# Kernel tuning notes

Measured on AMD Instinct MI355X. Metric: run time of the kernel, lower is better.

## Reference

```python
import jax, jax.numpy as jnp
import numpy as np

D, E, H, K = 1024, 8, 4096, 2
B, S = 4, 2048


def setup_inputs() -> dict:
    key = jax.random.key(0)
    ks = jax.random.split(key, 5)
    scale = 0.02
    return {
        "x": jax.random.normal(ks[0], (B, S, D), dtype=jnp.float32),
        "gate_w": jax.random.normal(ks[1], (D, E), dtype=jnp.float32) * scale,
        "w1": jax.random.normal(ks[2], (E, D, H), dtype=jnp.float32) * scale,
        "b1": jnp.zeros((E, H), dtype=jnp.float32),
        "w2": jax.random.normal(ks[3], (E, H, D), dtype=jnp.float32) * scale,
        "b2": jnp.zeros((E, D), dtype=jnp.float32),
        "top_k": K,
    }


def reference(x, gate_w, w1, b1, w2, b2, top_k):
    orig_shape = x.shape
    d = x.shape[-1]
    xt = x.reshape(-1, d)                      # [T, D]
    T = xt.shape[0]

    # Gating: top-k over expert scores, softmax over the selected k.
    scores = xt @ gate_w                       # [T, E]
    expert_weights, expert_indices = jax.lax.top_k(scores, top_k)  # [T, K]
    expert_weights = jax.nn.softmax(expert_weights, axis=-1)

    # Dense all-expert MLP (GPT-style fc -> GELU -> proj), batched over experts.
    h = jnp.einsum('td,edh->eth', xt, w1) + b1[:, None, :]   # [E, T, H]
    h = jax.nn.gelu(h, approximate=False)
    outs = jnp.einsum('eth,ehd->etd', h, w2) + b2[:, None, :]  # [E, T, D]

    # Combine: gather each token's selected experts and mix with gate weights.
    tok = jnp.arange(T)[:, None]               # [T, 1]
    gathered = outs[expert_indices, tok]       # [T, K, D]
    y = jnp.sum(gathered * expert_weights[..., None], axis=1)  # [T, D]
    return y.reshape(orig_shape)
```

## Files before the change

### kernel.cpp

```cpp
#include <hip/hip_runtime.h>
#include <stdint.h>

#define T_TOK 8192
#define D_DIM 1024
#define E_NUM 8
#define H_DIM 4096

#define BM 128
#define BN 128
#define BK 64
#define NSEG 8
#define MAX_ROWS2 17408
#define MAX_MT2 (MAX_ROWS2/BM)
#define LCS 136

typedef unsigned short u16;
typedef __attribute__((ext_vector_type(8))) short shortx8;
typedef __attribute__((ext_vector_type(4))) float floatx4;
typedef __attribute__((ext_vector_type(8))) unsigned short ushortx8;

typedef const __attribute__((address_space(1))) unsigned int g_uint;
typedef __attribute__((address_space(3))) unsigned int l_uint;

__device__ __forceinline__ u16 f2bf(float f) {
  union { float f; unsigned int u; } v; v.f = f;
  unsigned int r = v.u + 0x7FFFu + ((v.u >> 16) & 1u);
  return (u16)(r >> 16);
}
__device__ __forceinline__ void gld_lds16(const u16* g, u16* l) {
  __builtin_amdgcn_global_load_lds((g_uint*)g, (l_uint*)l, 16, 0, 0);
}
__device__ __forceinline__ float gelu_fast(float v) {
  float y = v * (1.5957691216f + 0.07135481627f * v * v);
  y = fminf(y, 30.f);
  float ey = __expf(y);
  return v * ey * __builtin_amdgcn_rcpf(1.f + ey);
}

__global__ __launch_bounds__(256) void init_kernel(int* counts, int* fills, int* row_token) {
  int i = blockIdx.x * 256 + threadIdx.x;
  if (i < MAX_ROWS2) row_token[i] = -1;
  if (blockIdx.x == 0 && threadIdx.x < NSEG) { counts[threadIdx.x] = 0; fills[threadIdx.x] = 0; }
}

__global__ __launch_bounds__(256) void zero4_kernel(float4* out) {
  out[(size_t)blockIdx.x * 256 + threadIdx.x] = float4{0.f, 0.f, 0.f, 0.f};
}

__global__ __launch_bounds__(256) void gate_kernel(const float* __restrict__ X, const float* __restrict__ GW,
                                                   u16* __restrict__ XC,
                                                   int* __restrict__ tk_idx, float* __restrict__ tk_w,
                                                   int* __restrict__ counts) {
  const int lane = threadIdx.x & 63;
  const int t = blockIdx.x * 4 + (threadIdx.x >> 6);
  const float4* xr4 = (const float4*)(X + (size_t)t * D_DIM + lane * 16);
  const float4* gw4 = (const float4*)GW;
  float acc[E_NUM];
#pragma unroll
  for (int e = 0; e < E_NUM; e++) acc[e] = 0.f;
  ushortx8 o0, o1;
#pragma unroll
  for (int i4 = 0; i4 < 4; i4++) {
    float4 xv = xr4[i4];
#pragma unroll
    for (int c = 0; c < 4; c++) {
      float xs = (&xv.x)[c];
      int q = i4 * 4 + c;
      if (q < 8) o0[q] = f2bf(xs); else o1[q - 8] = f2bf(xs);
      int d = lane * 16 + q;
      float4 g0 = gw4[d * 2], g1 = gw4[d * 2 + 1];
      acc[0] += xs * g0.x; acc[1] += xs * g0.y; acc[2] += xs * g0.z; acc[3] += xs * g0.w;
      acc[4] += xs * g1.x; acc[5] += xs * g1.y; acc[6] += xs * g1.z; acc[7] += xs * g1.w;
    }
  }
  u16* xcb = XC + (size_t)t * D_DIM + lane * 16;
  *(ushortx8*)xcb = o0;
  *(ushortx8*)(xcb + 8) = o1;
#pragma unroll
  for (int e = 0; e < E_NUM; e++)
    for (int off = 32; off; off >>= 1) acc[e] += __shfl_xor(acc[e], off);
  if (lane == 0) {
    int i0 = 0; float v0 = acc[0];
#pragma unroll
    for (int e = 1; e < E_NUM; e++) if (acc[e] > v0) { v0 = acc[e]; i0 = e; }
    int i1 = -1; float v1 = -1e30f;
#pragma unroll
    for (int e = 0; e < E_NUM; e++) if (e != i0 && acc[e] > v1) { v1 = acc[e]; i1 = e; }
    float e1 = expf(v1 - v0);
    float inv = 1.f / (1.f + e1);
    tk_idx[t * 2] = i0; tk_idx[t * 2 + 1] = i1;
    tk_w[t * 2] = inv;  tk_w[t * 2 + 1] = e1 * inv;
    atomicAdd(&counts[i0], 1); atomicAdd(&counts[i1], 1);
  }
}

__global__ void prefix_kernel(const int* counts, int* seg) {
  if (threadIdx.x == 0 && blockIdx.x == 0) {
    int a = 0;
    for (int i = 0; i < NSEG; i++) { seg[i] = a; a += ((counts[i] + BM - 1) / BM) * BM; }
    seg[NSEG] = a;
  }
}

__global__ __launch_bounds__(256) void fill_kernel(const int* __restrict__ tk_idx, const float* __restrict__ tk_w,
                                                   const int* __restrict__ seg, int* __restrict__ fills,
                                                   int* __restrict__ row_token, float* __restrict__ row_weight,
                                                   int* __restrict__ row_of) {
  int t = blockIdx.x * 256 + threadIdx.x;
  if (t >= T_TOK) return;
#pragma unroll
  for (int s = 0; s < 2; s++) {
    int sidx = tk_idx[t * 2 + s];
    int pos = atomicAdd(&fills[sidx], 1);
    int r = seg[sidx] + pos;
    row_token[r] = t; row_weight[r] = tk_w[t * 2 + s];
    row_of[t * 2 + s] = r;
  }
}

__global__ __launch_bounds__(256) void transpose_kernel(const float* __restrict__ src, u16* __restrict__ dst,
                                                        int R, int C) {
  __shared__ u16 tile[64][70];
  const int tid = threadIdx.x;
  size_t off = (size_t)blockIdx.z * (size_t)R * C;
  int r0 = blockIdx.y * 64, c0 = blockIdx.x * 64;
  int rr = tid >> 4, cc = (tid & 15) * 4;
#pragma unroll
  for (int i = 0; i < 4; i++) {
    int r = rr + i * 16;
    float4 v = *(const float4*)&src[off + (size_t)(r0 + r) * C + c0 + cc];
    u16* tp = &tile[r][cc];
    tp[0] = f2bf(v.x); tp[1] = f2bf(v.y); tp[2] = f2bf(v.z); tp[3] = f2bf(v.w);
  }
  __syncthreads();
  int c = tid >> 3, rb = (tid & 7) * 8;
#pragma unroll
  for (int i = 0; i < 2; i++) {
    int cx = c + i * 32;
    ushortx8 o;
#pragma unroll
    for (int q = 0; q < 8; q++) o[q] = tile[rb + q][cx];
    *(ushortx8*)&dst[off + (size_t)(c0 + cx) * R + r0 + rb] = o;
  }
}

__global__ __launch_bounds__(256, 4) void fc1_kernel(const u16* __restrict__ XC, const u16* __restrict__ W1T,
                                                     const float* __restrict__ B1, u16* __restrict__ Hbuf,
                                                     const int* __restrict__ row_token, const int* __restrict__ seg,
                                                     int mtile0, int e_filter) {
  const int ntile = blockIdx.x, mloc = blockIdx.y;
  const int mtile = mtile0 + mloc;
  const int row0 = mtile * BM;
  if (row0 >= seg[NSEG]) return;
  int sidx = 0;
#pragma unroll
  for (int i = 1; i < NSEG; i++) if (row0 >= seg[i]) sidx = i;
  const int e = sidx;
  if (e_filter >= 0 && e != e_filter) return;
  const size_t ebase = (e_filter >= 0) ? 0 : (size_t)e * H_DIM;
  const u16* Bbase = W1T + (ebase + (size_t)ntile * BN) * D_DIM;

  __shared__ u16 lds_u16[BM * LCS];
  u16* lA = lds_u16;
  u16* lB = lds_u16 + BM * BK;
  const int tid = threadIdx.x;
  const int sub = tid >> 3;
  const int csw = (((tid & 7) ^ (sub & 7)) * 8);
  unsigned int offA[4], offB[4];
#pragma unroll
  for (int r = 0; r < 4; r++) {
    int arow = r * 32 + sub;
    int tok = row_token[row0 + arow]; if (tok < 0) tok = 0;
    offA[r] = (unsigned int)tok * D_DIM + csw;
    offB[r] = (unsigned int)arow * D_DIM + csw;
  }
  const int lane = tid & 63;
  const int mq = (tid >> 7) & 1, nq = (tid >> 6) & 1;
  const int lrow = lane & 15, quad = lane >> 4;
  const int rsw = lrow & 7;
  floatx4 acc[4][4];
#pragma unroll
  for (int i = 0; i < 4; i++)
#pragma unroll
    for (int j = 0; j < 4; j++)
#pragma unroll
      for (int r = 0; r < 4; r++) acc[i][j][r] = 0.f;

  for (int k0 = 0; k0 < D_DIM; k0 += BK) {
#pragma unroll
    for (int r = 0; r < 4; r++) gld_lds16(XC + offA[r] + k0, &lA[(r * 256 + tid) * 8]);
#pragma unroll
    for (int r = 0; r < 4; r++) gld_lds16(Bbase + offB[r] + k0, &lB[(r * 256 + tid) * 8]);
    __syncthreads();
#pragma unroll
    for (int kk = 0; kk < 2; kk++) {
      const int ch = ((kk * 4 + quad) ^ rsw) * 8;
      shortx8 af[4], bfr[4];
#pragma unroll
      for (int i = 0; i < 4; i++) af[i]  = *(const shortx8*)&lA[(mq * 64 + i * 16 + lrow) * BK + ch];
#pragma unroll
      for (int i = 0; i < 4; i++) bfr[i] = *(const shortx8*)&lB[(nq * 64 + i * 16 + lrow) * BK + ch];
#pragma unroll
      for (int i = 0; i < 4; i++)
#pragma unroll
        for (int j = 0; j < 4; j++)
          acc[i][j] = __builtin_amdgcn_mfma_f32_16x16x32_bf16(af[i], bfr[j], acc[i][j], 0, 0, 0);
    }
    __syncthreads();
  }
#pragma unroll
  for (int j = 0; j < 4; j++) {
    float bv = B1[(size_t)e * H_DIM + ntile * BN + nq * 64 + j * 16 + lrow];
    int col = nq * 64 + j * 16 + lrow;
#pragma unroll
    for (int i = 0; i < 4; i++) {
      int row = mq * 64 + i * 16 + quad * 4;
#pragma unroll
      for (int rr = 0; rr < 4; rr++) {
        float v = acc[i][j][rr] + bv;
        lds_u16[(row + rr) * LCS + col] = f2bf(gelu_fast(v));
      }
    }
  }
  __syncthreads();
  {
    const int r = tid >> 1, c0 = (tid & 1) * 64;
    size_t gbase = (size_t)(mloc * BM + r) * H_DIM + (size_t)ntile * BN + c0;
#pragma unroll
    for (int q = 0; q < 8; q++)
      *(ushortx8*)&Hbuf[gbase + q * 8] = *(const ushortx8*)&lds_u16[r * LCS + c0 + q * 8];
  }
}

__global__ __launch_bounds__(256, 4) void fc2_kernel(const u16* __restrict__ Hbuf, const u16* __restrict__ W2T,
                                                     const float* __restrict__ B2, float* __restrict__ outbuf,
                                                     const int* __restrict__ row_token, const float* __restrict__ row_weight,
                                                     const int* __restrict__ seg,
                                                     int mtile0, int e_filter) {
  const int ntile = blockIdx.x, mloc = blockIdx.y;
  const int mtile = mtile0 + mloc;
  const int row0 = mtile * BM;
  if (row0 >= seg[NSEG]) return;
  int sidx = 0;
#pragma unroll
  for (int i = 1; i < NSEG; i++) if (row0 >= seg[i]) sidx = i;
  const int e = sidx;
  if (e_filter >= 0 && e != e_filter) return;
  const size_t ebase = (e_filter >= 0) ? 0 : (size_t)e * D_DIM;
  const u16* Bbase = W2T + (ebase + (size_t)ntile * BN) * H_DIM;

  __shared__ u16 lA[BM * BK];
  __shared__ u16 lB[BN * BK];
  const int tid = threadIdx.x;
  const int sub = tid >> 3;
  const int csw = (((tid & 7) ^ (sub & 7)) * 8);
  unsigned int offA[4], offB[4];
#pragma unroll
  for (int r = 0; r < 4; r++) {
    int arow = r * 32 + sub;
    offA[r] = (unsigned int)(mloc * BM + arow) * H_DIM + csw;
    offB[r] = (unsigned int)arow * H_DIM + csw;
  }
  const int lane = tid & 63;
  const int mq = (tid >> 7) & 1, nq = (tid >> 6) & 1;
  const int lrow = lane & 15, quad = lane >> 4;
  const int rsw = lrow & 7;
  floatx4 acc[4][4];
#pragma unroll
  for (int i = 0; i < 4; i++)
#pragma unroll
    for (int j = 0; j < 4; j++)
#pragma unroll
      for (int r = 0; r < 4; r++) acc[i][j][r] = 0.f;

  for (int k0 = 0; k0 < H_DIM; k0 += BK) {
#pragma unroll
    for (int r = 0; r < 4; r++) gld_lds16(Hbuf + offA[r] + k0, &lA[(r * 256 + tid) * 8]);
#pragma unroll
    for (int r = 0; r < 4; r++) gld_lds16(Bbase + offB[r] + k0, &lB[(r * 256 + tid) * 8]);
    __syncthreads();
#pragma unroll
    for (int kk = 0; kk < 2; kk++) {
      const int ch = ((kk * 4 + quad) ^ rsw) * 8;
      shortx8 af[4], bfr[4];
#pragma unroll
      for (int i = 0; i < 4; i++) af[i]  = *(const shortx8*)&lA[(mq * 64 + i * 16 + lrow) * BK + ch];
#pragma unroll
      for (int i = 0; i < 4; i++) bfr[i] = *(const shortx8*)&lB[(nq * 64 + i * 16 + lrow) * BK + ch];
#pragma unroll
      for (int i = 0; i < 4; i++)
#pragma unroll
        for (int j = 0; j < 4; j++)
          acc[i][j] = __builtin_amdgcn_mfma_f32_16x16x32_bf16(af[i], bfr[j], acc[i][j], 0, 0, 0);
    }
    __syncthreads();
  }
#pragma unroll
  for (int i = 0; i < 4; i++)
#pragma unroll
    for (int rr = 0; rr < 4; rr++) {
      int gr = row0 + mq * 64 + i * 16 + quad * 4 + rr;
      int tok = row_token[gr];
      if (tok >= 0) {
        float wgt = row_weight[gr];
        float* obase = outbuf + (size_t)gr * D_DIM + (size_t)ntile * BN + nq * 64 + lrow;
#pragma unroll
        for (int j = 0; j < 4; j++) {
          float bv = B2[(size_t)e * D_DIM + ntile * BN + nq * 64 + j * 16 + lrow];
          obase[j * 16] = (acc[i][j][rr] + bv) * wgt;
        }
      }
    }
}

__global__ __launch_bounds__(256) void combine_kernel(const float* __restrict__ outbuf, const int* __restrict__ row_of,
                                                      float* __restrict__ out) {
  int t = blockIdx.x;
  int d = threadIdx.x * 4;
  int r0 = row_of[t * 2], r1 = row_of[t * 2 + 1];
  float4 a = *(const float4*)&outbuf[(size_t)r0 * D_DIM + d];
  float4 b = *(const float4*)&outbuf[(size_t)r1 * D_DIM + d];
  *(float4*)&out[(size_t)t * D_DIM + d] = float4{a.x + b.x, a.y + b.y, a.z + b.z, a.w + b.w};
}

extern "C" void kernel_launch(void* const* d_in, const int* in_sizes, int n_in,
                              void* d_out, int out_size, void* d_ws, size_t ws_size,
                              hipStream_t stream) {
  const float* x  = (const float*)d_in[0];
  const float* gw = (const float*)d_in[1];
  const float* w1 = (const float*)d_in[2];
  const float* b1 = (const float*)d_in[3];
  const float* w2 = (const float*)d_in[4];
  const float* b2 = (const float*)d_in[5];
  float* out = (float*)d_out;

  char* p = (char*)d_ws;
  auto alloc = [&](size_t n) { char* q = p; p += (n + 255) & ~(size_t)255; return q; };
  int*   counts     = (int*)alloc(NSEG * 4);
  int*   fills      = (int*)alloc(NSEG * 4);
  int*   seg        = (int*)alloc((NSEG + 1) * 4);
  int*   tk_idx     = (int*)alloc((size_t)T_TOK * 2 * 4);
  float* tk_w       = (float*)alloc((size_t)T_TOK * 2 * 4);
  int*   row_token  = (int*)alloc((size_t)MAX_ROWS2 * 4);
  float* row_weight = (float*)alloc((size_t)MAX_ROWS2 * 4);
  int*   row_of     = (int*)alloc((size_t)T_TOK * 2 * 4);
  u16*   xc         = (u16*)alloc((size_t)T_TOK * D_DIM * 2);
  float* outbuf     = (float*)alloc((size_t)MAX_ROWS2 * D_DIM * 4);
  size_t meta = (size_t)(p - (char*)d_ws);

  const size_t Wfull = (size_t)E_NUM * H_DIM * D_DIM * 2;
  const size_t Wone  = (size_t)H_DIM * D_DIM * 2;
  auto hbytes = [](int n) { int cmx = (MAX_MT2 + n - 1) / n; return (size_t)cmx * BM * H_DIM * 2; };

  int mode = 3, N = 1;
  {
    const int cand[6] = {1, 2, 4, 8, 16, 32};
    for (int ci = 0; ci < 6 && mode == 3; ci++)
      if (meta + 2 * Wfull + hbytes(cand[ci]) <= ws_size) { mode = 0; N = cand[ci]; }
    for (int ci = 0; ci < 6 && mode == 3; ci++)
      if (meta + Wfull + hbytes(cand[ci]) <= ws_size) { mode = 1; N = cand[ci]; }
    for (int ci = 0; ci < 6 && mode == 3; ci++)
      if (meta + Wone + hbytes(cand[ci]) <= ws_size) { mode = 2; N = cand[ci]; }
  }

  if (mode == 3) {
    zero4_kernel<<<(int)(((size_t)T_TOK * D_DIM) / 1024), 256, 0, stream>>>((float4*)out);
    return;
  }

  u16 *W1T, *W2T;
  if (mode == 0) { W1T = (u16*)alloc(Wfull); W2T = (u16*)alloc(Wfull); }
  else           { W1T = W2T = (u16*)alloc(mode == 1 ? Wfull : Wone); }
  u16* Hbuf = (u16*)alloc(hbytes(N));
  const int cm = (MAX_MT2 + N - 1) / N;

  init_kernel<<<(MAX_ROWS2 + 255) / 256, 256, 0, stream>>>(counts, fills, row_token);
  gate_kernel<<<T_TOK / 4, 256, 0, stream>>>(x, gw, xc, tk_idx, tk_w, counts);
  prefix_kernel<<<1, 64, 0, stream>>>(counts, seg);
  fill_kernel<<<T_TOK / 256, 256, 0, stream>>>(tk_idx, tk_w, seg, fills, row_token, row_weight, row_of);

  if (mode == 0) {
    transpose_kernel<<<dim3(H_DIM / 64, D_DIM / 64, E_NUM), 256, 0, stream>>>(w1, W1T, D_DIM, H_DIM);
    transpose_kernel<<<dim3(D_DIM / 64, H_DIM / 64, E_NUM), 256, 0, stream>>>(w2, W2T, H_DIM, D_DIM);
  }

  for (int c = 0; c < N; ++c) {
    int mtile0 = c * cm;
    int cmc = MAX_MT2 - mtile0; if (cmc > cm) cmc = cm; if (cmc <= 0) break;
    if (mode == 0) {
      fc1_kernel<<<dim3(H_DIM / BN, cmc), 256, 0, stream>>>(xc, W1T, b1, Hbuf, row_token, seg, mtile0, -1);
      fc2_kernel<<<dim3(D_DIM / BN, cmc), 256, 0, stream>>>(Hbuf, W2T, b2, outbuf, row_token, row_weight, seg, mtile0, -1);
    } else if (mode == 1) {
      transpose_kernel<<<dim3(H_DIM / 64, D_DIM / 64, E_NUM), 256, 0, stream>>>(w1, W1T, D_DIM, H_DIM);
      fc1_kernel<<<dim3(H_DIM / BN, cmc), 256, 0, stream>>>(xc, W1T, b1, Hbuf, row_token, seg, mtile0, -1);
      transpose_kernel<<<dim3(D_DIM / 64, H_DIM / 64, E_NUM), 256, 0, stream>>>(w2, W2T, H_DIM, D_DIM);
      fc2_kernel<<<dim3(D_DIM / BN, cmc), 256, 0, stream>>>(Hbuf, W2T, b2, outbuf, row_token, row_weight, seg, mtile0, -1);
    } else {
      for (int e = 0; e < E_NUM; e++) {
        transpose_kernel<<<dim3(H_DIM / 64, D_DIM / 64, 1), 256, 0, stream>>>(w1 + (size_t)e * D_DIM * H_DIM, W1T, D_DIM, H_DIM);
        fc1_kernel<<<dim3(H_DIM / BN, cmc), 256, 0, stream>>>(xc, W1T, b1, Hbuf, row_token, seg, mtile0, e);
      }
      for (int e = 0; e < E_NUM; e++) {
        transpose_kernel<<<dim3(D_DIM / 64, H_DIM / 64, 1), 256, 0, stream>>>(w2 + (size_t)e * H_DIM * D_DIM, W2T, H_DIM, D_DIM);
        fc2_kernel<<<dim3(D_DIM / BN, cmc), 256, 0, stream>>>(Hbuf, W2T, b2, outbuf, row_token, row_weight, seg, mtile0, e);
      }
    }
  }
  combine_kernel<<<T_TOK, 256, 0, stream>>>(outbuf, row_of, out);
}
```

Measured before the change: 981.5 us.

## Double-buffer LDS tiles in fc1/fc2 GEMMs and merge weight transposes

The fc1 and fc2 GEMM main loops now use two LDS buffers. The next K-tile's global-to-LDS loads are issued before computing on the current one, with explicit vmcnt waits and raw s_barrier instead of __syncthreads. This overlaps memory latency with MFMA work, but doubles shared memory to 64KB per block, so the launch bound drops from 4 to 2 blocks per CU. The two weight transpose launches are also merged into one kernel to save a launch.

```diff
diff --git a/kernel.cpp b/kernel.cpp
--- a/kernel.cpp
+++ b/kernel.cpp
@@ -144,7 +144,41 @@
   }
 }
 
-__global__ __launch_bounds__(256, 4) void fc1_kernel(const u16* __restrict__ XC, const u16* __restrict__ W1T,
+__global__ __launch_bounds__(256) void transpose_all_kernel(const float* __restrict__ w1, const float* __restrict__ w2,
+                                                            u16* __restrict__ W1T, u16* __restrict__ W2T) {
+  __shared__ u16 tile[64][70];
+  const int tid = threadIdx.x;
+  const int z = blockIdx.y;
+  const bool is1 = z < E_NUM;
+  const int e = is1 ? z : z - E_NUM;
+  const int C = is1 ? H_DIM : D_DIM;
+  const float* src = (is1 ? w1 : w2) + (size_t)e * D_DIM * H_DIM;
+  u16* dst = (is1 ? W1T : W2T) + (size_t)e * D_DIM * H_DIM;
+  const int ncx = C >> 6;
+  const int flat = blockIdx.x;
+  int c0 = (flat & (ncx - 1)) * 64, r0 = (flat / ncx) * 64;
+  int rr = tid >> 4, cc = (tid & 15) * 4;
+#pragma unroll
+  for (int i = 0; i < 4; i++) {
+    int r = rr + i * 16;
+    float4 v = *(const float4*)&src[(size_t)(r0 + r) * C + c0 + cc];
+    u16* tp = &tile[r][cc];
+    tp[0] = f2bf(v.x); tp[1] = f2bf(v.y); tp[2] = f2bf(v.z); tp[3] = f2bf(v.w);
+  }
+  __syncthreads();
+  const int R = is1 ? D_DIM : H_DIM;
+  int c = tid >> 3, rb = (tid & 7) * 8;
+#pragma unroll
+  for (int i = 0; i < 2; i++) {
+    int cx = c + i * 32;
+    ushortx8 o;
+#pragma unroll
+    for (int q = 0; q < 8; q++) o[q] = tile[rb + q][cx];
+    *(ushortx8*)&dst[(size_t)(c0 + cx) * R + r0 + rb] = o;
+  }
+}
+
+__global__ __launch_bounds__(256, 2) void fc1_kernel(const u16* __restrict__ XC, const u16* __restrict__ W1T,
                                                      const float* __restrict__ B1, u16* __restrict__ Hbuf,
                                                      const int* __restrict__ row_token, const int* __restrict__ seg,
                                                      int mtile0, int e_filter) {
@@ -160,9 +194,7 @@
   const size_t ebase = (e_filter >= 0) ? 0 : (size_t)e * H_DIM;
   const u16* Bbase = W1T + (ebase + (size_t)ntile * BN) * D_DIM;
 
-  __shared__ u16 lds_u16[BM * LCS];
-  u16* lA = lds_u16;
-  u16* lB = lds_u16 + BM * BK;
+  __shared__ u16 lds[32768];
   const int tid = threadIdx.x;
   const int sub = tid >> 3;
   const int csw = (((tid & 7) ^ (sub & 7)) * 8);
@@ -186,27 +218,40 @@
 #pragma unroll
       for (int r = 0; r < 4; r++) acc[i][j][r] = 0.f;
 
+  auto stage = [&](int k0, int b) {
+    u16* la = &lds[b * 16384];
+    u16* lb = la + 8192;
+#pragma unroll
+    for (int r = 0; r < 4; r++) gld_lds16(XC + offA[r] + k0, &la[(r * 256 + tid) * 8]);
+#pragma unroll
+    for (int r = 0; r < 4; r++) gld_lds16(Bbase + offB[r] + k0, &lb[(r * 256 + tid) * 8]);
+  };
+  stage(0, 0);
+  int buf = 0;
   for (int k0 = 0; k0 < D_DIM; k0 += BK) {
-#pragma unroll
-    for (int r = 0; r < 4; r++) gld_lds16(XC + offA[r] + k0, &lA[(r * 256 + tid) * 8]);
-#pragma unroll
-    for (int r = 0; r < 4; r++) gld_lds16(Bbase + offB[r] + k0, &lB[(r * 256 + tid) * 8]);
-    __syncthreads();
+    if (k0 + BK < D_DIM) { stage(k0 + BK, buf ^ 1); asm volatile("s_waitcnt vmcnt(8)" ::: "memory"); }
+    else                 { asm volatile("s_waitcnt vmcnt(0)" ::: "memory"); }
+    __builtin_amdgcn_s_barrier();
+    __builtin_amdgcn_sched_barrier(0);
+    const u16* la = &lds[buf * 16384];
+    const u16* lb = la + 8192;
 #pragma unroll
     for (int kk = 0; kk < 2; kk++) {
       const int ch = ((kk * 4 + quad) ^ rsw) * 8;
       shortx8 af[4], bfr[4];
 #pragma unroll
-      for (int i = 0; i < 4; i++) af[i]  = *(const shortx8*)&lA[(mq * 64 + i * 16 + lrow) * BK + ch];
-#pragma unroll
-      for (int i = 0; i < 4; i++) bfr[i] = *(const shortx8*)&lB[(nq * 64 + i * 16 + lrow) * BK + ch];
+      for (int i = 0; i < 4; i++) af[i]  = *(const shortx8*)&la[(mq * 64 + i * 16 + lrow) * BK + ch];
+#pragma unroll
+      for (int i = 0; i < 4; i++) bfr[i] = *(const shortx8*)&lb[(nq * 64 + i * 16 + lrow) * BK + ch];
 #pragma unroll
       for (int i = 0; i < 4; i++)
 #pragma unroll
         for (int j = 0; j < 4; j++)
           acc[i][j] = __builtin_amdgcn_mfma_f32_16x16x32_bf16(af[i], bfr[j], acc[i][j], 0, 0, 0);
     }
-    __syncthreads();
+    __builtin_amdgcn_sched_barrier(0);
+    __builtin_amdgcn_s_barrier();
+    buf ^= 1;
   }
 #pragma unroll
   for (int j = 0; j < 4; j++) {
@@ -218,7 +263,7 @@
 #pragma unroll
       for (int rr = 0; rr < 4; rr++) {
         float v = acc[i][j][rr] + bv;
-        lds_u16[(row + rr) * LCS + col] = f2bf(gelu_fast(v));
+        lds[(row + rr) * LCS + col] = f2bf(gelu_fast(v));
       }
     }
   }
@@ -228,11 +273,11 @@
     size_t gbase = (size_t)(mloc * BM + r) * H_DIM + (size_t)ntile * BN + c0;
 #pragma unroll
     for (int q = 0; q < 8; q++)
-      *(ushortx8*)&Hbuf[gbase + q * 8] = *(const ushortx8*)&lds_u16[r * LCS + c0 + q * 8];
-  }
-}
-
-__global__ __launch_bounds__(256, 4) void fc2_kernel(const u16* __restrict__ Hbuf, const u16* __restrict__ W2T,
+      *(ushortx8*)&Hbuf[gbase + q * 8] = *(const ushortx8*)&lds[r * LCS + c0 + q * 8];
+  }
+}
+
+__global__ __launch_bounds__(256, 2) void fc2_kernel(const u16* __restrict__ Hbuf, const u16* __restrict__ W2T,
                                                      const float* __restrict__ B2, float* __restrict__ outbuf,
                                                      const int* __restrict__ row_token, const float* __restrict__ row_weight,
                                                      const int* __restrict__ seg,
@@ -249,8 +294,7 @@
   const size_t ebase = (e_filter >= 0) ? 0 : (size_t)e * D_DIM;
   const u16* Bbase = W2T + (ebase + (size_t)ntile * BN) * H_DIM;
 
-  __shared__ u16 lA[BM * BK];
-  __shared__ u16 lB[BN * BK];
+  __shared__ u16 lds[32768];
   const int tid = threadIdx.x;
   const int sub = tid >> 3;
   const int csw = (((tid & 7) ^ (sub & 7)) * 8);
@@ -273,27 +317,40 @@
 #pragma unroll
       for (int r = 0; r < 4; r++) acc[i][j][r] = 0.f;
 
+  auto stage = [&](int k0, int b) {
+    u16* la = &lds[b * 16384];
+    u16* lb = la + 8192;
+#pragma unroll
+    for (int r = 0; r < 4; r++) gld_lds16(Hbuf + offA[r] + k0, &la[(r * 256 + tid) * 8]);
+#pragma unroll
+    for (int r = 0; r < 4; r++) gld_lds16(Bbase + offB[r] + k0, &lb[(r * 256 + tid) * 8]);
+  };
+  stage(0, 0);
+  int buf = 0;
   for (int k0 = 0; k0 < H_DIM; k0 += BK) {
-#pragma unroll
-    for (int r = 0; r < 4; r++) gld_lds16(Hbuf + offA[r] + k0, &lA[(r * 256 + tid) * 8]);
-#pragma unroll
-    for (int r = 0; r < 4; r++) gld_lds16(Bbase + offB[r] + k0, &lB[(r * 256 + tid) * 8]);
-    __syncthreads();
+    if (k0 + BK < H_DIM) { stage(k0 + BK, buf ^ 1); asm volatile("s_waitcnt vmcnt(8)" ::: "memory"); }
+    else                 { asm volatile("s_waitcnt vmcnt(0)" ::: "memory"); }
+    __builtin_amdgcn_s_barrier();
+    __builtin_amdgcn_sched_barrier(0);
+    const u16* la = &lds[buf * 16384];
+    const u16* lb = la + 8192;
 #pragma unroll
     for (int kk = 0; kk < 2; kk++) {
       const int ch = ((kk * 4 + quad) ^ rsw) * 8;
       shortx8 af[4], bfr[4];
 #pragma unroll
-      for (int i = 0; i < 4; i++) af[i]  = *(const shortx8*)&lA[(mq * 64 + i * 16 + lrow) * BK + ch];
-#pragma unroll
-      for (int i = 0; i < 4; i++) bfr[i] = *(const shortx8*)&lB[(nq * 64 + i * 16 + lrow) * BK + ch];
+      for (int i = 0; i < 4; i++) af[i]  = *(const shortx8*)&la[(mq * 64 + i * 16 + lrow) * BK + ch];
+#pragma unroll
+      for (int i = 0; i < 4; i++) bfr[i] = *(const shortx8*)&lb[(nq * 64 + i * 16 + lrow) * BK + ch];
 #pragma unroll
       for (int i = 0; i < 4; i++)
 #pragma unroll
         for (int j = 0; j < 4; j++)
           acc[i][j] = __builtin_amdgcn_mfma_f32_16x16x32_bf16(af[i], bfr[j], acc[i][j], 0, 0, 0);
     }
-    __syncthreads();
+    __builtin_amdgcn_sched_barrier(0);
+    __builtin_amdgcn_s_barrier();
+    buf ^= 1;
   }
 #pragma unroll
   for (int i = 0; i < 4; i++)
@@ -380,8 +437,7 @@
   fill_kernel<<<T_TOK / 256, 256, 0, stream>>>(tk_idx, tk_w, seg, fills, row_token, row_weight, row_of);
 
   if (mode == 0) {
-    transpose_kernel<<<dim3(H_DIM / 64, D_DIM / 64, E_NUM), 256, 0, stream>>>(w1, W1T, D_DIM, H_DIM);
-    transpose_kernel<<<dim3(D_DIM / 64, H_DIM / 64, E_NUM), 256, 0, stream>>>(w2, W2T, H_DIM, D_DIM);
+    transpose_all_kernel<<<dim3(1024, 2 * E_NUM), 256, 0, stream>>>(w1, w2, W1T, W2T);
   }
 
   for (int c = 0; c < N; ++c) {
```

After: 988.1 us. About the same (+0.7%).
